# Optimization experiments

Hardware: AMD Instinct MI355X
Metric: run time of the kernel (lower is better)

Reference implementation:

```python
import jax, jax.numpy as jnp
import numpy as np

NEG = -1e15  # matches mask_logits constant -1000000000000000.0


def setup_inputs() -> dict:
    key = jax.random.key(0)
    ks = jax.random.split(key, 4)
    B, d, c_len, q_len = 64, 512, 1024, 128
    C = jax.random.normal(ks[0], (B, d, c_len), dtype=jnp.float32)
    Q = jax.random.normal(ks[1], (B, d, q_len), dtype=jnp.float32)
    c_mask = jnp.ones((B, c_len), dtype=jnp.float32)
    q_mask = jnp.ones((B, q_len), dtype=jnp.float32)
    W0 = jax.random.normal(ks[2], (3 * d,), dtype=jnp.float32) / np.sqrt(d).astype(np.float32)
    Wr = jax.random.normal(ks[3], (d, 4 * d), dtype=jnp.float32) * np.float32(0.02)
    return {"C": C, "Q": Q, "c_mask": c_mask, "q_mask": q_mask, "W0": W0, "Wr": Wr}


def reference(C, Q, c_mask, q_mask, W0, Wr):
    # C: [B, d, c], Q: [B, d, q]
    d = C.shape[1]
    C_t = jnp.swapaxes(C, 1, 2)  # [B, c, d]
    Q_t = jnp.swapaxes(Q, 1, 2)  # [B, q, d]
    w_c, w_q, w_m = W0[:d], W0[d:2 * d], W0[2 * d:]
    # Trilinear similarity, algebraically identical to cat([C,Q,C*Q]) @ W0
    S = (C_t @ w_c)[:, :, None] + (Q_t @ w_q)[:, None, :] \
        + jnp.einsum('bid,bjd->bij', C_t * w_m, Q_t)  # [B, c, q]
    qm = q_mask[:, None, :]  # [B, 1, q]
    cm = c_mask[:, :, None]  # [B, c, 1]
    S_bar = jax.nn.softmax(S * qm + NEG * (1.0 - qm), axis=2)
    S_bbar = jax.nn.softmax(S * cm + NEG * (1.0 - cm), axis=1)
    A = S_bar @ Q_t  # [B, c, d]
    Bm = jnp.einsum('bij,bkj->bik', S_bar, S_bbar) @ C_t  # [B, c, d]
    out = jnp.concatenate([C_t, A, C_t * A, C_t * Bm], axis=2)  # [B, c, 4d]
    # dropout inactive (eval mode); 1x1 conv == matmul with Wr [d, 4d]
    return jnp.einsum('od,bcd->boc', Wr, out)  # [B, d, c]
```

## Files before the change

kernel.cpp:

```cpp
#include <hip/hip_runtime.h>
#include <hip/hip_bf16.h>

typedef unsigned short u16;
typedef __attribute__((ext_vector_type(8))) short short8;
typedef __attribute__((ext_vector_type(4))) short short4v;
typedef __attribute__((ext_vector_type(4))) float f32x4;

#define NEGV -1000000000000000.0f
#define SBAR() asm volatile("s_barrier" ::: "memory")

__device__ __forceinline__ u16 f2bf(float f) {
  unsigned u = __float_as_uint(f);
  unsigned r = (u + 0x7FFFu + ((u >> 16) & 1u)) >> 16;
  return (u16)r;
}
__device__ __forceinline__ float bf2f(u16 s) {
  return __uint_as_float(((unsigned)s) << 16);
}
__device__ __forceinline__ void lds16(const void* g, void* l) {
  __builtin_amdgcn_global_load_lds((const __attribute__((address_space(1))) void*)g,
                                   (__attribute__((address_space(3))) void*)l,
                                   16, 0, 0);
}

__global__ __launch_bounds__(1024) void gemm8b(const u16* __restrict__ A,
                                               const u16* __restrict__ B,
                                               float* __restrict__ out) {
  extern __shared__ u16 lds[];
  const int bid = blockIdx.x;
  const int wg = (bid & 7) * 64 + (bid >> 3);
  const int m0 = (wg & 1) * 256;
  const int n0 = (wg >> 1) * 256;
  const int tid = threadIdx.x;
  const int lane = tid & 63;
  const int w = tid >> 6;
  const int wr = w >> 2;
  const int wc = w & 3;
  const int fro = lane & 15;
  const int hi = lane >> 4;
  const int kx = fro & 7;
  const int sr = lane >> 3;
  const int sgc = ((lane & 7) ^ sr) << 3;

  const u16* Ag = A + (size_t)m0 * 2048;
  const u16* Bg = B + (size_t)n0 * 2048;
  const int rA = wr * 64 + fro;
  const int rB = wc * 64 + fro;

  f32x4 acc[4][4] = {};

#define STG(gp, lp) \
  lds16((gp) + (size_t)(w * 8 + sr) * 2048 + sgc, (u16*)(lp) + w * 512)
#define RDF(base, row, k16) \
  (*(const short8*)&(base)[(size_t)(row) * 64 + (((k16) ^ kx) << 3)])

  STG(Ag, lds);
  STG(Ag + 262144, lds + 8192);
  STG(Bg, lds + 32768);
  STG(Bg + 262144, lds + 32768 + 8192);
  STG(Bg + 64, lds + 49152);
  STG(Bg + 262144 + 64, lds + 49152 + 8192);
  asm volatile("s_waitcnt vmcnt(2)" ::: "memory");
  SBAR();

  const u16* Ac = lds;
  u16* An = lds + 16384;
  const u16* Bc = lds + 32768;
  const u16* Bn = lds + 49152;
  u16* Bs2 = lds + 65536;

  for (int t = 0; t < 32; ++t) {
    const int kkA = (t < 31 ? t + 1 : 31) * 64;
    const int kkB = (t < 30 ? t + 2 : 31) * 64;
    short8 af[4], bf[4];

#pragma unroll
    for (int i = 0; i < 4; ++i) af[i] = RDF(Ac, rA + i * 16, hi);
#pragma unroll
    for (int j = 0; j < 4; ++j) bf[j] = RDF(Bc, rB + j * 16, hi);
    STG(Ag + kkA, An);
    STG(Ag + 262144 + kkA, An + 8192);
    SBAR();
    __builtin_amdgcn_s_setprio(1);
#pragma unroll
    for (int i = 0; i < 4; ++i)
#pragma unroll
      for (int j = 0; j < 4; ++j)
        acc[i][j] =
            __builtin_amdgcn_mfma_f32_16x16x32_bf16(af[i], bf[j], acc[i][j], 0, 0, 0);
    __builtin_amdgcn_s_setprio(0);
    SBAR();

#pragma unroll
    for (int i = 0; i < 4; ++i) af[i] = RDF(Ac, rA + i * 16, 4 + hi);
#pragma unroll
    for (int j = 0; j < 4; ++j) bf[j] = RDF(Bc, rB + j * 16, 4 + hi);
    STG(Bg + kkB, Bs2);
    STG(Bg + 262144 + kkB, Bs2 + 8192);
    asm volatile("s_waitcnt vmcnt(2)" ::: "memory");
    SBAR();
    __builtin_amdgcn_s_setprio(1);
#pragma unroll
    for (int i = 0; i < 4; ++i)
#pragma unroll
      for (int j = 0; j < 4; ++j)
        acc[i][j] =
            __builtin_amdgcn_mfma_f32_16x16x32_bf16(af[i], bf[j], acc[i][j], 0, 0, 0);
    __builtin_amdgcn_s_setprio(0);
    SBAR();

    u16* tA = An; An = (u16*)Ac; Ac = tA;
    u16* tB = (u16*)Bc; Bc = Bn; Bn = Bs2; Bs2 = tB;
  }
  asm volatile("s_waitcnt vmcnt(0)" ::: "memory");

  const int crow = m0 + wr * 64 + hi * 4;
#pragma unroll
  for (int i = 0; i < 4; ++i)
#pragma unroll
    for (int j = 0; j < 4; ++j) {
      const int n = n0 + wc * 64 + j * 16 + fro;
      float* op = out + (size_t)(n >> 10) * 524288 + (n & 1023);
#pragma unroll
      for (int g = 0; g < 4; ++g)
        op[(size_t)(crow + i * 16 + g) * 1024] = acc[i][j][g];
    }
#undef STG
#undef RDF
}

__global__ __launch_bounds__(256) void gemm_t(const u16* __restrict__ A,
                                              const u16* __restrict__ B,
                                              const float* __restrict__ csum,
                                              u16* __restrict__ Tt) {
  __shared__ u16 As[128 * 64];
  __shared__ u16 Bs[128 * 64];
  const int b = blockIdx.z;
  const int n0 = blockIdx.y * 128;
  const u16* Ab = A + (size_t)b * 131072;
  const u16* Bb = B + (size_t)b * 524288;
  const int t = threadIdx.x;
  const int lane = t & 63;
  const int w = t >> 6;
  const int wr = w >> 1, wc = w & 1;
  const int srow = lane >> 3;
  const int scol = (lane & 7) * 8;

  f32x4 acc[4][4] = {};

  for (int k0 = 0; k0 < 1024; k0 += 64) {
    __syncthreads();
#pragma unroll
    for (int qq = 0; qq < 4; ++qq) {
      const int q = w * 4 + qq;
      const int r = q * 8 + srow;
      lds16(Ab + (size_t)r * 1024 + k0 + scol, &As[q * 512]);
      lds16(Bb + (size_t)(n0 + r) * 1024 + k0 + scol, &Bs[q * 512]);
    }
    __syncthreads();
#pragma unroll
    for (int ks = 0; ks < 2; ++ks) {
      short8 af[4], bg[4];
      const int fro = lane & 15;
      const int k8 = ks * 32 + (lane >> 4) * 8;
#pragma unroll
      for (int i = 0; i < 4; ++i)
        af[i] = *(const short8*)&As[(wr * 64 + i * 16 + fro) * 64 + k8];
#pragma unroll
      for (int i = 0; i < 4; ++i)
        bg[i] = *(const short8*)&Bs[(wc * 64 + i * 16 + fro) * 64 + k8];
#pragma unroll
      for (int i = 0; i < 4; ++i)
#pragma unroll
        for (int j = 0; j < 4; ++j)
          acc[i][j] =
              __builtin_amdgcn_mfma_f32_16x16x32_bf16(af[i], bg[j], acc[i][j], 0, 0, 0);
    }
  }

  const int col = lane & 15;
  const int r4 = (lane >> 4) * 4;
#pragma unroll
  for (int i = 0; i < 4; ++i)
#pragma unroll
    for (int g = 0; g < 4; ++g) {
      const int rr = wr * 64 + i * 16 + r4 + g;
      const float inv = 1.f / csum[b * 128 + rr];
#pragma unroll
      for (int j = 0; j < 4; ++j) {
        const int cc = n0 + wc * 64 + j * 16 + col;
        Tt[(size_t)b * 65536 + (size_t)cc * 128 + rr] = f2bf(acc[i][j][g] * inv);
      }
    }
}

__global__ __launch_bounds__(256) void gemm_s(
    const u16* __restrict__ A, const u16* __restrict__ Bq,
    const float* __restrict__ cb, const float* __restrict__ qb,
    const float* __restrict__ cmask, const float* __restrict__ qmask,
    u16* __restrict__ Sbar, u16* __restrict__ EunT, float* __restrict__ csum) {
  __shared__ u16 As[128 * 64];
  __shared__ u16 Bs[128 * 64];
  __shared__ u16 Lt[128][136];
  __shared__ float rmaxs[2][128];
  __shared__ float rsums[2][128];
  __shared__ float cparts[2][128];
  const int b = blockIdx.z;
  const int m0 = blockIdx.x * 128;
  const u16* Ab = A + (size_t)b * 2097152;
  const u16* Bb = Bq + (size_t)b * 65536;
  const int t = threadIdx.x;
  const int lane = t & 63;
  const int w = t >> 6;
  const int wr = w >> 1, wc = w & 1;
  const int srow = lane >> 3;
  const int scol = (lane & 7) * 8;

  f32x4 acc[4][4] = {};

  for (int k0 = 0; k0 < 512; k0 += 64) {
    __syncthreads();
#pragma unroll
    for (int qq = 0; qq < 4; ++qq) {
      const int q = w * 4 + qq;
      const int r = q * 8 + srow;
      lds16(Ab + (size_t)(m0 + r) * 2048 + k0 + scol, &As[q * 512]);
      lds16(Bb + (size_t)r * 512 + k0 + scol, &Bs[q * 512]);
    }
    __syncthreads();
#pragma unroll
    for (int ks = 0; ks < 2; ++ks) {
      short8 af[4], bg[4];
      const int fro = lane & 15;
      const int k8 = ks * 32 + (lane >> 4) * 8;
#pragma unroll
      for (int i = 0; i < 4; ++i)
        af[i] = *(const short8*)&As[(wr * 64 + i * 16 + fro) * 64 + k8];
#pragma unroll
      for (int i = 0; i < 4; ++i)
        bg[i] = *(const short8*)&Bs[(wc * 64 + i * 16 + fro) * 64 + k8];
#pragma unroll
      for (int i = 0; i < 4; ++i)
#pragma unroll
        for (int j = 0; j < 4; ++j)
          acc[i][j] =
              __builtin_amdgcn_mfma_f32_16x16x32_bf16(af[i], bg[j], acc[i][j], 0, 0, 0);
    }
  }

  const int fro = lane & 15;
  const int hi = lane >> 4;
  float qv[4], qbv[4];
#pragma unroll
  for (int j = 0; j < 4; ++j) {
    const int cc = wc * 64 + j * 16 + fro;
    qv[j] = qmask[b * 128 + cc];
    qbv[j] = qb[b * 128 + cc];
  }
  float colp[4] = {0.f, 0.f, 0.f, 0.f};
#pragma unroll
  for (int i = 0; i < 4; ++i)
#pragma unroll
    for (int g = 0; g < 4; ++g) {
      const int rl = wr * 64 + i * 16 + hi * 4 + g;
      const float rb = cb[b * 1024 + m0 + rl];
      const float cv = cmask[b * 1024 + m0 + rl];
      const float coff = NEGV * (1.f - cv);
#pragma unroll
      for (int j = 0; j < 4; ++j) {
        const float v = acc[i][j][g] + rb + qbv[j];
        acc[i][j][g] = v;
        const float e = __expf(v * cv + coff);
        Lt[wc * 64 + j * 16 + fro][rl] = f2bf(e);
        colp[j] += e;
      }
    }
#pragma unroll
  for (int j = 0; j < 4; ++j) {
    colp[j] += __shfl_xor(colp[j], 16);
    colp[j] += __shfl_xor(colp[j], 32);
  }
  if (hi == 0)
#pragma unroll
    for (int j = 0; j < 4; ++j) cparts[wr][wc * 64 + j * 16 + fro] = colp[j];
  float rtmp[4][4];
#pragma unroll
  for (int i = 0; i < 4; ++i)
#pragma unroll
    for (int g = 0; g < 4; ++g) {
      float m = -3.4e38f;
#pragma unroll
      for (int j = 0; j < 4; ++j) {
        const float xm = acc[i][j][g] * qv[j] + NEGV * (1.f - qv[j]);
        acc[i][j][g] = xm;
        m = fmaxf(m, xm);
      }
#pragma unroll
      for (int o = 8; o; o >>= 1) m = fmaxf(m, __shfl_xor(m, o));
      rtmp[i][g] = m;
    }
  if (fro == 0)
#pragma unroll
    for (int i = 0; i < 4; ++i)
#pragma unroll
      for (int g = 0; g < 4; ++g)
        rmaxs[wc][wr * 64 + i * 16 + hi * 4 + g] = rtmp[i][g];
  __syncthreads();
  if (t < 128) atomicAdd(&csum[b * 128 + t], cparts[0][t] + cparts[1][t]);
  {
    const int jr = t >> 1;
    const int ih = (t & 1) * 64;
    u16* dst = EunT + (size_t)b * 131072 + (size_t)jr * 1024 + m0 + ih;
#pragma unroll
    for (int s = 0; s < 8; ++s)
      *(short8*)(dst + s * 8) = *(const short8*)&Lt[jr][ih + s * 8];
  }
#pragma unroll
  for (int i = 0; i < 4; ++i)
#pragma unroll
    for (int g = 0; g < 4; ++g) {
      const int rl = wr * 64 + i * 16 + hi * 4 + g;
      const float M = fmaxf(rmaxs[0][rl], rmaxs[1][rl]);
      float s = 0.f;
#pragma unroll
      for (int j = 0; j < 4; ++j) {
        const float p = __expf(acc[i][j][g] - M);
        acc[i][j][g] = p;
        s += p;
      }
#pragma unroll
      for (int o = 8; o; o >>= 1) s += __shfl_xor(s, o);
      rtmp[i][g] = s;
    }
  if (fro == 0)
#pragma unroll
    for (int i = 0; i < 4; ++i)
#pragma unroll
      for (int g = 0; g < 4; ++g)
        rsums[wc][wr * 64 + i * 16 + hi * 4 + g] = rtmp[i][g];
  __syncthreads();
#pragma unroll
  for (int i = 0; i < 4; ++i)
#pragma unroll
    for (int g = 0; g < 4; ++g) {
      const int rl = wr * 64 + i * 16 + hi * 4 + g;
      const float inv = 1.f / (rsums[0][rl] + rsums[1][rl]);
#pragma unroll
      for (int j = 0; j < 4; ++j)
        Sbar[((size_t)b * 1024 + m0 + rl) * 128 + wc * 64 + j * 16 + fro] =
            f2bf(acc[i][j][g] * inv);
    }
}

__global__ __launch_bounds__(256) void gemm_ab(const u16* __restrict__ Sbar,
                                               const u16* __restrict__ Qo,
                                               const u16* __restrict__ Tt,
                                               u16* __restrict__ O) {
  __shared__ u16 sh[3 * 128 * 64];
  u16* As = sh;
  u16* Bq = sh + 8192;
  u16* Bt = sh + 16384;
  const int b = blockIdx.z;
  const int m0 = blockIdx.x * 128;
  const int dcol = blockIdx.y * 128;
  const u16* Ab = Sbar + (size_t)b * 131072;
  const u16* Qg = Qo + (size_t)b * 65536 + (size_t)dcol * 128;
  const u16* Tg = Tt + (size_t)b * 65536 + (size_t)dcol * 128;
  const int t = threadIdx.x;
  const int lane = t & 63;
  const int w = t >> 6;
  const int wr = w >> 1, wc = w & 1;
  const int srow = lane >> 3;
  const int scol = (lane & 7) * 8;
  const int fro = lane & 15;
  const int hi = lane >> 4;

  f32x4 aa[4][4] = {};
  f32x4 ab[4][4] = {};

  for (int k0 = 0; k0 < 128; k0 += 64) {
    __syncthreads();
#pragma unroll
    for (int qq = 0; qq < 4; ++qq) {
      const int q = w * 4 + qq;
      const int r = q * 8 + srow;
      lds16(Ab + (size_t)(m0 + r) * 128 + k0 + scol, &As[q * 512]);
      lds16(Qg + (size_t)r * 128 + k0 + scol, &Bq[q * 512]);
      lds16(Tg + (size_t)r * 128 + k0 + scol, &Bt[q * 512]);
    }
    __syncthreads();
#pragma unroll
    for (int ks = 0; ks < 2; ++ks) {
      short8 af[4], bq[4], bt[4];
      const int k8 = ks * 32 + hi * 8;
#pragma unroll
      for (int i = 0; i < 4; ++i) {
        af[i] = *(const short8*)&As[(wr * 64 + i * 16 + fro) * 64 + k8];
        bq[i] = *(const short8*)&Bq[(wc * 64 + i * 16 + fro) * 64 + k8];
        bt[i] = *(const short8*)&Bt[(wc * 64 + i * 16 + fro) * 64 + k8];
      }
#pragma unroll
      for (int i = 0; i < 4; ++i)
#pragma unroll
        for (int j = 0; j < 4; ++j) {
          aa[i][j] =
              __builtin_amdgcn_mfma_f32_16x16x32_bf16(af[i], bq[j], aa[i][j], 0, 0, 0);
          ab[i][j] =
              __builtin_amdgcn_mfma_f32_16x16x32_bf16(af[i], bt[j], ab[i][j], 0, 0, 0);
        }
    }
  }

  u16* Ls = sh;
  const int erow = t >> 4;
  const int ecol = (t & 15) * 8;
  const size_t obase0 = (size_t)b * 2097152 + (size_t)m0 * 2048 + dcol;
  short8 c8[8];

  __syncthreads();
#pragma unroll
  for (int i = 0; i < 4; ++i)
#pragma unroll
    for (int j = 0; j < 4; ++j)
#pragma unroll
      for (int g = 0; g < 4; ++g)
        Ls[(wr * 64 + i * 16 + hi * 4 + g) * 128 + wc * 64 + j * 16 + fro] =
            f2bf(aa[i][j][g]);
  __syncthreads();
#pragma unroll
  for (int it = 0; it < 8; ++it) {
    const int row = it * 16 + erow;
    const short8 a8 = *(const short8*)&Ls[row * 128 + ecol];
    c8[it] = *(const short8*)&O[obase0 + (size_t)row * 2048 + ecol];
    short8 p2;
#pragma unroll
    for (int k = 0; k < 8; ++k)
      p2[k] = (short)f2bf(bf2f((u16)c8[it][k]) * bf2f((u16)a8[k]));
    *(short8*)&O[obase0 + (size_t)row * 2048 + ecol + 512] = a8;
    *(short8*)&O[obase0 + (size_t)row * 2048 + ecol + 1024] = p2;
  }
  __syncthreads();
#pragma unroll
  for (int i = 0; i < 4; ++i)
#pragma unroll
    for (int j = 0; j < 4; ++j)
#pragma unroll
      for (int g = 0; g < 4; ++g)
        Ls[(wr * 64 + i * 16 + hi * 4 + g) * 128 + wc * 64 + j * 16 + fro] =
            f2bf(ab[i][j][g]);
  __syncthreads();
#pragma unroll
  for (int it = 0; it < 8; ++it) {
    const int row = it * 16 + erow;
    const short8 b8 = *(const short8*)&Ls[row * 128 + ecol];
    short8 p3;
#pragma unroll
    for (int k = 0; k < 8; ++k)
      p3[k] = (short)f2bf(bf2f((u16)c8[it][k]) * bf2f((u16)b8[k]));
    *(short8*)&O[obase0 + (size_t)row * 2048 + ecol + 1536] = p3;
  }
}

__global__ __launch_bounds__(256) void prep_C(const float* __restrict__ C,
                                              const float* __restrict__ W0,
                                              u16* __restrict__ O,
                                              u16* __restrict__ Corig,
                                              float* __restrict__ cb) {
  __shared__ float L[64][65];
  __shared__ float P[4][64];
  const int b = blockIdx.z;
  const int d0 = blockIdx.y * 64;
  const int i0 = blockIdx.x * 64;
  const int t = threadIdx.x;
  const int cx = t & 63;
  const int rb = t >> 6;
  const float* Cb = C + ((size_t)b * 512 + d0) * 1024 + i0;
  float part = 0.f;
#pragma unroll
  for (int rr = 0; rr < 16; ++rr) {
    const int r = rb * 16 + rr;
    const float v = Cb[(size_t)r * 1024 + cx];
    L[r][cx] = v;
    part = fmaf(v, W0[d0 + r], part);
    Corig[((size_t)b * 512 + d0 + r) * 1024 + i0 + cx] = f2bf(v);
  }
  P[rb][cx] = part;
  __syncthreads();
#pragma unroll
  for (int rr = 0; rr < 16; ++rr) {
    const int il = rb * 16 + rr;
    O[((size_t)b * 1024 + i0 + il) * 2048 + d0 + cx] = f2bf(L[cx][il]);
  }
  if (rb == 0)
    atomicAdd(&cb[b * 1024 + i0 + cx], P[0][cx] + P[1][cx] + P[2][cx] + P[3][cx]);
}

__global__ __launch_bounds__(256) void prep_Q(const float* __restrict__ Q,
                                              const float* __restrict__ W0,
                                              u16* __restrict__ Qmb,
                                              u16* __restrict__ Qorig,
                                              float* __restrict__ qb) {
  __shared__ float L[64][65];
  __shared__ float P[4][64];
  const int b = blockIdx.z;
  const int d0 = blockIdx.y * 64;
  const int j0 = blockIdx.x * 64;
  const int t = threadIdx.x;
  const int cx = t & 63;
  const int rb = t >> 6;
  const float* Qb = Q + ((size_t)b * 512 + d0) * 128 + j0;
  float part = 0.f;
#pragma unroll
  for (int rr = 0; rr < 16; ++rr) {
    const int r = rb * 16 + rr;
    const float v = Qb[(size_t)r * 128 + cx];
    L[r][cx] = v;
    part = fmaf(v, W0[512 + d0 + r], part);
    Qorig[((size_t)b * 512 + d0 + r) * 128 + j0 + cx] = f2bf(v);
  }
  P[rb][cx] = part;
  __syncthreads();
  const float wm = W0[1024 + d0 + cx];
#pragma unroll
  for (int rr = 0; rr < 16; ++rr) {
    const int jl = rb * 16 + rr;
    Qmb[((size_t)b * 128 + j0 + jl) * 512 + d0 + cx] = f2bf(L[cx][jl] * wm);
  }
  if (rb == 0)
    atomicAdd(&qb[b * 128 + j0 + cx], P[0][cx] + P[1][cx] + P[2][cx] + P[3][cx]);
}

__global__ __launch_bounds__(256) void cvt_wr(const float* __restrict__ Wr,
                                              u16* __restrict__ Wrb) {
  const int idx = blockIdx.x * 256 + threadIdx.x;
  const float4 v = ((const float4*)Wr)[idx];
  short4v o;
  o[0] = (short)f2bf(v.x);
  o[1] = (short)f2bf(v.y);
  o[2] = (short)f2bf(v.z);
  o[3] = (short)f2bf(v.w);
  *(short4v*)&Wrb[(size_t)idx * 4] = o;
}

extern "C" void kernel_launch(void* const* d_in, const int* in_sizes, int n_in,
                              void* d_out, int out_size, void* d_ws, size_t ws_size,
                              hipStream_t stream) {
  (void)in_sizes; (void)n_in; (void)out_size;
  const float* C = (const float*)d_in[0];
  const float* Q = (const float*)d_in[1];
  const float* cm = (const float*)d_in[2];
  const float* qm = (const float*)d_in[3];
  const float* W0 = (const float*)d_in[4];
  const float* Wr = (const float*)d_in[5];
  float* out = (float*)d_out;

  if (ws_size < 405078016ull) return;

  char* p = (char*)d_ws;
  u16* O     = (u16*)(p);
  u16* Corig = (u16*)(p + 268435456ull);
  u16* Qmb   = (u16*)(p + 335544320ull);
  u16* Qorig = (u16*)(p + 343932928ull);
  u16* EunT  = (u16*)(p + 360710144ull);
  u16* Sbar  = (u16*)(p + 377487360ull);
  u16* Tt    = (u16*)(p + 394264576ull);
  u16* Wrb   = (u16*)(p + 402653184ull);
  float* cb  = (float*)(p + 404750336ull);
  float* qb  = (float*)(p + 405012480ull);
  float* csum= (float*)(p + 405045248ull);

  hipFuncSetAttribute((const void*)gemm8b,
                      hipFuncAttributeMaxDynamicSharedMemorySize, 163840);
  hipMemsetAsync(cb, 0, 327680, stream);

  cvt_wr<<<dim3(1024), dim3(256), 0, stream>>>(Wr, Wrb);
  prep_C<<<dim3(16, 8, 64), dim3(256), 0, stream>>>(C, W0, O, Corig, cb);
  prep_Q<<<dim3(2, 8, 64), dim3(256), 0, stream>>>(Q, W0, Qmb, Qorig, qb);

  gemm_s<<<dim3(8, 1, 64), dim3(256), 0, stream>>>(O, Qmb, cb, qb, cm, qm,
                                                   Sbar, EunT, csum);

  gemm_t<<<dim3(1, 4, 64), dim3(256), 0, stream>>>(EunT, Corig, csum, Tt);

  gemm_ab<<<dim3(8, 4, 64), dim3(256), 0, stream>>>(Sbar, Qorig, Tt, O);

  gemm8b<<<dim3(512), dim3(1024), 163840, stream>>>(Wrb, O, out);
}
```

Before: 368.4 us.

## Replace 256x256 final GEMM with 128x128 tiles, 4-stage ring, LDS-staged stores

Rewrites the final output-projection GEMM. It drops the single large 1024-thread, 256x256-tile workgroup in favour of 256-thread workgroups on 128x128 tiles with two blocks per CU. Each K step is 32 wide and fed by a 4-deep LDS ring with one barrier per step. The accumulator is staged through LDS so the output can be written with coalesced float4 row stores instead of strided scalar stores. The smaller tiles increase occupancy and parallelism but reduce operand reuse, which raises global and LDS traffic per FLOP.

Result: slower. 464.4 us (+26.1%).

```diff
diff --git a/kernel.cpp b/kernel.cpp
--- a/kernel.cpp
+++ b/kernel.cpp
@@ -23,64 +23,64 @@
                                    16, 0, 0);
 }
 
-__global__ __launch_bounds__(1024) void gemm8b(const u16* __restrict__ A,
-                                               const u16* __restrict__ B,
-                                               float* __restrict__ out) {
+__global__ __launch_bounds__(256, 2) void gemm_w(const u16* __restrict__ A,
+                                                 const u16* __restrict__ B,
+                                                 float* __restrict__ out) {
   extern __shared__ u16 lds[];
   const int bid = blockIdx.x;
-  const int wg = (bid & 7) * 64 + (bid >> 3);
-  const int m0 = (wg & 1) * 256;
-  const int n0 = (wg >> 1) * 256;
+  const int xcd = bid & 7;
+  const int k = bid >> 3;
+  const int nl = k >> 2;
+  const int m0 = (k & 3) * 128;
+  const int nf = (xcd * 64 + nl) * 128;
   const int tid = threadIdx.x;
   const int lane = tid & 63;
   const int w = tid >> 6;
-  const int wr = w >> 2;
-  const int wc = w & 3;
-  const int fro = lane & 15;
-  const int hi = lane >> 4;
-  const int kx = fro & 7;
-  const int sr = lane >> 3;
-  const int sgc = ((lane & 7) ^ sr) << 3;
+  const int wr = w >> 1, wc = w & 1;
+  const int fro = lane & 15, hi = lane >> 4;
+  const int srow = tid >> 2;
+  const int sslot = tid & 3;
 
   const u16* Ag = A + (size_t)m0 * 2048;
-  const u16* Bg = B + (size_t)n0 * 2048;
+  const u16* Bg = B + (size_t)nf * 2048;
   const int rA = wr * 64 + fro;
   const int rB = wc * 64 + fro;
 
   f32x4 acc[4][4] = {};
 
-#define STG(gp, lp) \
-  lds16((gp) + (size_t)(w * 8 + sr) * 2048 + sgc, (u16*)(lp) + w * 512)
-#define RDF(base, row, k16) \
-  (*(const short8*)&(base)[(size_t)(row) * 64 + (((k16) ^ kx) << 3)])
-
-  STG(Ag, lds);
-  STG(Ag + 262144, lds + 8192);
-  STG(Bg, lds + 32768);
-  STG(Bg + 262144, lds + 32768 + 8192);
-  STG(Bg + 64, lds + 49152);
-  STG(Bg + 262144 + 64, lds + 49152 + 8192);
-  asm volatile("s_waitcnt vmcnt(2)" ::: "memory");
+#define STG(gp, k0, lp)                                                        \
+  {                                                                            \
+    lds16((gp) + (size_t)srow * 2048 + (k0) + ((sslot ^ (srow & 3)) << 3),     \
+          (u16*)(lp) + tid * 8);                                               \
+    lds16((gp) + (size_t)(64 + srow) * 2048 + (k0) +                           \
+              ((sslot ^ (srow & 3)) << 3),                                     \
+          (u16*)(lp) + 2048 + tid * 8);                                        \
+  }
+#define RDF(lp, row)                                                           \
+  (*(const short8*)&((const u16*)(lp))[(size_t)(row) * 32 +                    \
+                                       ((hi ^ ((row) & 3)) << 3)])
+
+  STG(Ag, 0, lds);
+  STG(Bg, 0, lds + 16384);
+  STG(Ag, 32, lds + 4096);
+  STG(Bg, 32, lds + 16384 + 4096);
+  asm volatile("s_waitcnt vmcnt(4)" ::: "memory");
   SBAR();
 
-  const u16* Ac = lds;
-  u16* An = lds + 16384;
-  const u16* Bc = lds + 32768;
-  const u16* Bn = lds + 49152;
-  u16* Bs2 = lds + 65536;
-
-  for (int t = 0; t < 32; ++t) {
-    const int kkA = (t < 31 ? t + 1 : 31) * 64;
-    const int kkB = (t < 30 ? t + 2 : 31) * 64;
+  for (int t = 0; t < 64; ++t) {
+    const int q2 = (t + 2) & 3;
+    const int kk = (t < 62 ? t + 2 : 63) * 32;
+    STG(Ag, kk, lds + q2 * 4096);
+    STG(Bg, kk, lds + 16384 + q2 * 4096);
+    asm volatile("s_waitcnt vmcnt(4)" ::: "memory");
+    SBAR();
+    const u16* La = lds + (t & 3) * 4096;
+    const u16* Lb = lds + 16384 + (t & 3) * 4096;
     short8 af[4], bf[4];
-
-#pragma unroll
-    for (int i = 0; i < 4; ++i) af[i] = RDF(Ac, rA + i * 16, hi);
-#pragma unroll
-    for (int j = 0; j < 4; ++j) bf[j] = RDF(Bc, rB + j * 16, hi);
-    STG(Ag + kkA, An);
-    STG(Ag + 262144 + kkA, An + 8192);
-    SBAR();
+#pragma unroll
+    for (int i = 0; i < 4; ++i) af[i] = RDF(La, rA + i * 16);
+#pragma unroll
+    for (int j = 0; j < 4; ++j) bf[j] = RDF(Lb, rB + j * 16);
     __builtin_amdgcn_s_setprio(1);
 #pragma unroll
     for (int i = 0; i < 4; ++i)
@@ -89,42 +89,28 @@
         acc[i][j] =
             __builtin_amdgcn_mfma_f32_16x16x32_bf16(af[i], bf[j], acc[i][j], 0, 0, 0);
     __builtin_amdgcn_s_setprio(0);
-    SBAR();
-
-#pragma unroll
-    for (int i = 0; i < 4; ++i) af[i] = RDF(Ac, rA + i * 16, 4 + hi);
-#pragma unroll
-    for (int j = 0; j < 4; ++j) bf[j] = RDF(Bc, rB + j * 16, 4 + hi);
-    STG(Bg + kkB, Bs2);
-    STG(Bg + 262144 + kkB, Bs2 + 8192);
-    asm volatile("s_waitcnt vmcnt(2)" ::: "memory");
-    SBAR();
-    __builtin_amdgcn_s_setprio(1);
-#pragma unroll
-    for (int i = 0; i < 4; ++i)
-#pragma unroll
-      for (int j = 0; j < 4; ++j)
-        acc[i][j] =
-            __builtin_amdgcn_mfma_f32_16x16x32_bf16(af[i], bf[j], acc[i][j], 0, 0, 0);
-    __builtin_amdgcn_s_setprio(0);
-    SBAR();
-
-    u16* tA = An; An = (u16*)Ac; Ac = tA;
-    u16* tB = (u16*)Bc; Bc = Bn; Bn = Bs2; Bs2 = tB;
   }
   asm volatile("s_waitcnt vmcnt(0)" ::: "memory");
-
-  const int crow = m0 + wr * 64 + hi * 4;
+  SBAR();
+
+  float* Lf = (float*)lds;
 #pragma unroll
   for (int i = 0; i < 4; ++i)
 #pragma unroll
     for (int j = 0; j < 4; ++j) {
-      const int n = n0 + wc * 64 + j * 16 + fro;
-      float* op = out + (size_t)(n >> 10) * 524288 + (n & 1023);
+      const int col = wc * 64 + j * 16 + fro;
 #pragma unroll
       for (int g = 0; g < 4; ++g)
-        op[(size_t)(crow + i * 16 + g) * 1024] = acc[i][j][g];
-    }
+        Lf[(wr * 64 + i * 16 + hi * 4 + g) * 132 + col] = acc[i][j][g];
+    }
+  __syncthreads();
+  const int row = tid >> 1;
+  const int ch = (tid & 1) * 64;
+  float* orow = out + (size_t)(nf >> 10) * 524288 + (size_t)(m0 + row) * 1024 +
+                (nf & 1023) + ch;
+#pragma unroll
+  for (int q = 0; q < 16; ++q)
+    *(float4*)(orow + q * 4) = *(float4*)&Lf[row * 132 + ch + q * 4];
 #undef STG
 #undef RDF
 }
@@ -434,8 +420,8 @@
     c8[it] = *(const short8*)&O[obase0 + (size_t)row * 2048 + ecol];
     short8 p2;
 #pragma unroll
-    for (int k = 0; k < 8; ++k)
-      p2[k] = (short)f2bf(bf2f((u16)c8[it][k]) * bf2f((u16)a8[k]));
+    for (int kk = 0; kk < 8; ++kk)
+      p2[kk] = (short)f2bf(bf2f((u16)c8[it][kk]) * bf2f((u16)a8[kk]));
     *(short8*)&O[obase0 + (size_t)row * 2048 + ecol + 512] = a8;
     *(short8*)&O[obase0 + (size_t)row * 2048 + ecol + 1024] = p2;
   }
@@ -455,8 +441,8 @@
     const short8 b8 = *(const short8*)&Ls[row * 128 + ecol];
     short8 p3;
 #pragma unroll
-    for (int k = 0; k < 8; ++k)
-      p3[k] = (short)f2bf(bf2f((u16)c8[it][k]) * bf2f((u16)b8[k]));
+    for (int kk = 0; kk < 8; ++kk)
+      p3[kk] = (short)f2bf(bf2f((u16)c8[it][kk]) * bf2f((u16)b8[kk]));
     *(short8*)&O[obase0 + (size_t)row * 2048 + ecol + 1536] = p3;
   }
 }
@@ -569,8 +555,8 @@
   float* qb  = (float*)(p + 405012480ull);
   float* csum= (float*)(p + 405045248ull);
 
-  hipFuncSetAttribute((const void*)gemm8b,
-                      hipFuncAttributeMaxDynamicSharedMemorySize, 163840);
+  hipFuncSetAttribute((const void*)gemm_w,
+                      hipFuncAttributeMaxDynamicSharedMemorySize, 67584);
   hipMemsetAsync(cb, 0, 327680, stream);
 
   cvt_wr<<<dim3(1024), dim3(256), 0, stream>>>(Wr, Wrb);
@@ -584,5 +570,5 @@
 
   gemm_ab<<<dim3(8, 4, 64), dim3(256), 0, stream>>>(Sbar, Qorig, Tt, O);
 
-  gemm8b<<<dim3(512), dim3(1024), 163840, stream>>>(Wrb, O, out);
-}
+  gemm_w<<<dim3(2048), dim3(256), 67584, stream>>>(Wrb, O, out);
+}
```

## Restructure A/B GEMM to keep Q and T tiles resident and double-buffer Sbar

Applied to the files above, without the earlier changes.

Replaces gemm_ab with gemm_ab2, which uses 512-thread blocks, one per (batch, 128-column d slice). Each block loads the full Q and T tiles into LDS once and loops over all eight 128-row chunks of Sbar, double-buffering the next chunk while computing the current one. LDS uses an XOR swizzle to avoid bank conflicts. This removes the repeated global reloads of Q/T tiles across m-blocks and covers load latency, at the cost of 160KB of dynamic LDS per block, a much smaller grid (256 blocks), and extra barriers per chunk.

After: 355.7 us. 1.04x faster.

```diff
diff --git a/kernel.cpp b/kernel.cpp
--- a/kernel.cpp
+++ b/kernel.cpp
@@ -352,113 +352,125 @@
     }
 }
 
-__global__ __launch_bounds__(256) void gemm_ab(const u16* __restrict__ Sbar,
-                                               const u16* __restrict__ Qo,
-                                               const u16* __restrict__ Tt,
-                                               u16* __restrict__ O) {
-  __shared__ u16 sh[3 * 128 * 64];
-  u16* As = sh;
-  u16* Bq = sh + 8192;
-  u16* Bt = sh + 16384;
-  const int b = blockIdx.z;
-  const int m0 = blockIdx.x * 128;
-  const int dcol = blockIdx.y * 128;
-  const u16* Ab = Sbar + (size_t)b * 131072;
-  const u16* Qg = Qo + (size_t)b * 65536 + (size_t)dcol * 128;
-  const u16* Tg = Tt + (size_t)b * 65536 + (size_t)dcol * 128;
+__global__ __launch_bounds__(512) void gemm_ab2(const u16* __restrict__ Sbar,
+                                                const u16* __restrict__ Qo,
+                                                const u16* __restrict__ Tt,
+                                                u16* __restrict__ O) {
+  extern __shared__ u16 sh[];
+  u16* LQ = sh;
+  u16* LT = sh + 16384;
+  u16* Ls = sh + 65536;
+  const int dcol = blockIdx.x * 128;
+  const int b = blockIdx.y;
   const int t = threadIdx.x;
   const int lane = t & 63;
   const int w = t >> 6;
-  const int wr = w >> 1, wc = w & 1;
-  const int srow = lane >> 3;
-  const int scol = (lane & 7) * 8;
-  const int fro = lane & 15;
-  const int hi = lane >> 4;
-
-  f32x4 aa[4][4] = {};
-  f32x4 ab[4][4] = {};
-
-  for (int k0 = 0; k0 < 128; k0 += 64) {
-    __syncthreads();
-#pragma unroll
-    for (int qq = 0; qq < 4; ++qq) {
-      const int q = w * 4 + qq;
-      const int r = q * 8 + srow;
-      lds16(Ab + (size_t)(m0 + r) * 128 + k0 + scol, &As[q * 512]);
-      lds16(Qg + (size_t)r * 128 + k0 + scol, &Bq[q * 512]);
-      lds16(Tg + (size_t)r * 128 + k0 + scol, &Bt[q * 512]);
-    }
-    __syncthreads();
-#pragma unroll
-    for (int ks = 0; ks < 2; ++ks) {
-      short8 af[4], bq[4], bt[4];
-      const int k8 = ks * 32 + hi * 8;
+  const int wr = w >> 2, wc = w & 3;
+  const int fro = lane & 15, hi = lane >> 4;
+  const int srow4 = t >> 4;
+  const int sslot = t & 15;
+
+  const u16* Qg = Qo + (size_t)b * 65536 + (size_t)dcol * 128;
+  const u16* Tg = Tt + (size_t)b * 65536 + (size_t)dcol * 128;
+  const u16* Sg = Sbar + (size_t)b * 131072;
+
+#define STG32(gp, lp)                                                         \
+  {                                                                           \
+    _Pragma("unroll") for (int ii = 0; ii < 4; ++ii) {                        \
+      const int row_ = ii * 32 + srow4;                                       \
+      lds16((gp) + (size_t)row_ * 128 + ((sslot ^ (row_ & 7)) << 3),          \
+            (u16*)(lp) + ii * 4096 + t * 8);                                  \
+    }                                                                         \
+  }
+#define RDS(base, row, kslot)                                                 \
+  (*(const short8*)&(base)[(size_t)(row) * 128 + (((kslot) ^ ((row) & 7)) << 3)])
+
+  STG32(Qg, LQ);
+  STG32(Tg, LT);
+  STG32(Sg, sh + 32768);
+  asm volatile("s_waitcnt vmcnt(0)" ::: "memory");
+  __syncthreads();
+
+  for (int mm = 0; mm < 8; ++mm) {
+    const u16* LSc = sh + 32768 + ((size_t)(mm & 1) << 14);
+    u16* LSn = sh + 32768 + ((size_t)((mm + 1) & 1) << 14);
+    if (mm < 7) STG32(Sg + (size_t)(mm + 1) * 16384, LSn);
+
+    f32x4 aa[4][2] = {};
+    f32x4 ab[4][2] = {};
+#pragma unroll
+    for (int ks = 0; ks < 4; ++ks) {
+      short8 af[4], bq[2], bt[2];
 #pragma unroll
       for (int i = 0; i < 4; ++i) {
-        af[i] = *(const short8*)&As[(wr * 64 + i * 16 + fro) * 64 + k8];
-        bq[i] = *(const short8*)&Bq[(wc * 64 + i * 16 + fro) * 64 + k8];
-        bt[i] = *(const short8*)&Bt[(wc * 64 + i * 16 + fro) * 64 + k8];
+        const int r = wr * 64 + i * 16 + fro;
+        af[i] = RDS(LSc, r, ks * 4 + hi);
       }
 #pragma unroll
+      for (int j = 0; j < 2; ++j) {
+        const int r = wc * 32 + j * 16 + fro;
+        bq[j] = RDS(LQ, r, ks * 4 + hi);
+        bt[j] = RDS(LT, r, ks * 4 + hi);
+      }
+#pragma unroll
       for (int i = 0; i < 4; ++i)
 #pragma unroll
-        for (int j = 0; j < 4; ++j) {
+        for (int j = 0; j < 2; ++j) {
           aa[i][j] =
               __builtin_amdgcn_mfma_f32_16x16x32_bf16(af[i], bq[j], aa[i][j], 0, 0, 0);
           ab[i][j] =
               __builtin_amdgcn_mfma_f32_16x16x32_bf16(af[i], bt[j], ab[i][j], 0, 0, 0);
         }
     }
-  }
-
-  u16* Ls = sh;
-  const int erow = t >> 4;
-  const int ecol = (t & 15) * 8;
-  const size_t obase0 = (size_t)b * 2097152 + (size_t)m0 * 2048 + dcol;
-  short8 c8[8];
-
-  __syncthreads();
-#pragma unroll
-  for (int i = 0; i < 4; ++i)
-#pragma unroll
-    for (int j = 0; j < 4; ++j)
-#pragma unroll
-      for (int g = 0; g < 4; ++g)
-        Ls[(wr * 64 + i * 16 + hi * 4 + g) * 128 + wc * 64 + j * 16 + fro] =
-            f2bf(aa[i][j][g]);
-  __syncthreads();
-#pragma unroll
-  for (int it = 0; it < 8; ++it) {
-    const int row = it * 16 + erow;
-    const short8 a8 = *(const short8*)&Ls[row * 128 + ecol];
-    c8[it] = *(const short8*)&O[obase0 + (size_t)row * 2048 + ecol];
-    short8 p2;
-#pragma unroll
-    for (int k = 0; k < 8; ++k)
-      p2[k] = (short)f2bf(bf2f((u16)c8[it][k]) * bf2f((u16)a8[k]));
-    *(short8*)&O[obase0 + (size_t)row * 2048 + ecol + 512] = a8;
-    *(short8*)&O[obase0 + (size_t)row * 2048 + ecol + 1024] = p2;
-  }
-  __syncthreads();
-#pragma unroll
-  for (int i = 0; i < 4; ++i)
-#pragma unroll
-    for (int j = 0; j < 4; ++j)
-#pragma unroll
-      for (int g = 0; g < 4; ++g)
-        Ls[(wr * 64 + i * 16 + hi * 4 + g) * 128 + wc * 64 + j * 16 + fro] =
-            f2bf(ab[i][j][g]);
-  __syncthreads();
-#pragma unroll
-  for (int it = 0; it < 8; ++it) {
-    const int row = it * 16 + erow;
-    const short8 b8 = *(const short8*)&Ls[row * 128 + ecol];
-    short8 p3;
-#pragma unroll
-    for (int k = 0; k < 8; ++k)
-      p3[k] = (short)f2bf(bf2f((u16)c8[it][k]) * bf2f((u16)b8[k]));
-    *(short8*)&O[obase0 + (size_t)row * 2048 + ecol + 1536] = p3;
-  }
+
+    const size_t obase = (size_t)b * 2097152 + (size_t)mm * 262144 + dcol;
+    __syncthreads();
+#pragma unroll
+    for (int i = 0; i < 4; ++i)
+#pragma unroll
+      for (int j = 0; j < 2; ++j)
+#pragma unroll
+        for (int g = 0; g < 4; ++g)
+          Ls[(wr * 64 + i * 16 + hi * 4 + g) * 128 + wc * 32 + j * 16 + fro] =
+              f2bf(aa[i][j][g]);
+    __syncthreads();
+    short8 c8[4];
+#pragma unroll
+    for (int it = 0; it < 4; ++it) {
+      const int row = it * 32 + srow4;
+      const short8 a8 = *(const short8*)&Ls[row * 128 + sslot * 8];
+      c8[it] = *(const short8*)&O[obase + (size_t)row * 2048 + sslot * 8];
+      short8 p2;
+#pragma unroll
+      for (int k = 0; k < 8; ++k)
+        p2[k] = (short)f2bf(bf2f((u16)c8[it][k]) * bf2f((u16)a8[k]));
+      *(short8*)&O[obase + (size_t)row * 2048 + sslot * 8 + 512] = a8;
+      *(short8*)&O[obase + (size_t)row * 2048 + sslot * 8 + 1024] = p2;
+    }
+    __syncthreads();
+#pragma unroll
+    for (int i = 0; i < 4; ++i)
+#pragma unroll
+      for (int j = 0; j < 2; ++j)
+#pragma unroll
+        for (int g = 0; g < 4; ++g)
+          Ls[(wr * 64 + i * 16 + hi * 4 + g) * 128 + wc * 32 + j * 16 + fro] =
+              f2bf(ab[i][j][g]);
+    __syncthreads();
+#pragma unroll
+    for (int it = 0; it < 4; ++it) {
+      const int row = it * 32 + srow4;
+      const short8 b8 = *(const short8*)&Ls[row * 128 + sslot * 8];
+      short8 p3;
+#pragma unroll
+      for (int k = 0; k < 8; ++k)
+        p3[k] = (short)f2bf(bf2f((u16)c8[it][k]) * bf2f((u16)b8[k]));
+      *(short8*)&O[obase + (size_t)row * 2048 + sslot * 8 + 1536] = p3;
+    }
+    __syncthreads();
+  }
+#undef STG32
+#undef RDS
 }
 
 __global__ __launch_bounds__(256) void prep_C(const float* __restrict__ C,
@@ -569,9 +581,11 @@
   float* qb  = (float*)(p + 405012480ull);
   float* csum= (float*)(p + 405045248ull);
 
-  hipFuncSetAttribute((const void*)gemm8b,
-                      hipFuncAttributeMaxDynamicSharedMemorySize, 163840);
-  hipMemsetAsync(cb, 0, 327680, stream);
+  (void)hipFuncSetAttribute((const void*)gemm8b,
+                            hipFuncAttributeMaxDynamicSharedMemorySize, 163840);
+  (void)hipFuncSetAttribute((const void*)gemm_ab2,
+                            hipFuncAttributeMaxDynamicSharedMemorySize, 163840);
+  (void)hipMemsetAsync(cb, 0, 327680, stream);
 
   cvt_wr<<<dim3(1024), dim3(256), 0, stream>>>(Wr, Wrb);
   prep_C<<<dim3(16, 8, 64), dim3(256), 0, stream>>>(C, W0, O, Corig, cb);
@@ -582,7 +596,7 @@
 
   gemm_t<<<dim3(1, 4, 64), dim3(256), 0, stream>>>(EunT, Corig, csum, Tt);
 
-  gemm_ab<<<dim3(8, 4, 64), dim3(256), 0, stream>>>(Sbar, Qorig, Tt, O);
+  gemm_ab2<<<dim3(4, 64), dim3(512), 163840, stream>>>(Sbar, Qorig, Tt, O);
 
   gemm8b<<<dim3(512), dim3(1024), 163840, stream>>>(Wrb, O, out);
 }
```
